# Kernel tuning notes

Measured on AMD Instinct MI355X. Metric: run time of the kernel, lower is better.

## Reference

```python
import jax, jax.numpy as jnp
import numpy as np

N_NODES = 50000
N_EDGES = 800000
D = 256
VOCAB = 50000
N_ETYPES = 3
N_STEPS = 5
N_GRAPHS = 64


def setup_inputs() -> dict:
    key = jax.random.key(0)
    ks = jax.random.split(key, 16)
    s = 1.0 / np.sqrt(D)
    return {
        "x": jax.random.randint(ks[0], (N_NODES,), 0, VOCAB),
        "src": jax.random.randint(ks[1], (N_EDGES,), 0, N_NODES),
        "dst": jax.random.randint(ks[2], (N_EDGES,), 0, N_NODES),
        "etypes": jax.random.randint(ks[3], (N_EDGES,), 0, N_ETYPES),
        "seg_ids": jnp.sort(jax.random.randint(ks[4], (N_NODES,), 0, N_GRAPHS)),
        "num_graphs": N_GRAPHS,
        "emb": jax.random.normal(ks[5], (VOCAB, D), jnp.float32),
        "W_msg": jax.random.normal(ks[6], (N_ETYPES, D, D), jnp.float32) * s,
        "b_msg": jax.random.normal(ks[7], (N_ETYPES, D), jnp.float32) * s,
        "w_ih": jax.random.normal(ks[8], (3 * D, D), jnp.float32) * s,
        "w_hh": jax.random.normal(ks[9], (3 * D, D), jnp.float32) * s,
        "b_ih": jax.random.normal(ks[10], (3 * D,), jnp.float32) * s,
        "b_hh": jax.random.normal(ks[11], (3 * D,), jnp.float32) * s,
        "gate_w": jax.random.normal(ks[12], (D, 1), jnp.float32) * s,
        "gate_b": jax.random.normal(ks[13], (1,), jnp.float32) * s,
    }


def _gru_cell(a, h, w_ih, w_hh, b_ih, b_hh):
    # a, h: [N, D]; gates: [N, 3D]
    gi = a @ w_ih.T + b_ih
    gh = h @ w_hh.T + b_hh
    i_r, i_z, i_n = jnp.split(gi, 3, axis=-1)
    h_r, h_z, h_n = jnp.split(gh, 3, axis=-1)
    r = jax.nn.sigmoid(i_r + h_r)
    z = jax.nn.sigmoid(i_z + h_z)
    n = jnp.tanh(i_n + r * h_n)
    return (1.0 - z) * n + z * h


def reference(x, src, dst, etypes, seg_ids, num_graphs, emb, W_msg, b_msg,
              w_ih, w_hh, b_ih, b_hh, gate_w, gate_b):
    # Embedding lookup (dropout is identity in eval mode)
    h = emb[x]  # [N, D]

    # GatedGraphConv: n_steps of per-etype linear message + scatter-add + GRU
    for _ in range(N_STEPS):
        # per-node transform under every etype's weight: [n_etypes, N, D]
        t = jnp.einsum("nd,edf->enf", h, W_msg)
        msg = t[etypes, src] + b_msg[etypes]        # [E, D]
        a = jax.ops.segment_sum(msg, dst, num_segments=N_NODES)  # [N, D]
        h = _gru_cell(a, h, w_ih, w_hh, b_ih, b_hh)

    # GlobalAttentionPooling: gate score + segment softmax + weighted sum
    gate = (h @ gate_w + gate_b)[:, 0]  # [N]
    gmax = jax.ops.segment_max(gate, seg_ids, num_segments=num_graphs)
    e = jnp.exp(gate - gmax[seg_ids])
    denom = jax.ops.segment_sum(e, seg_ids, num_segments=num_graphs)
    alpha = e / denom[seg_ids]  # [N]
    out = jax.ops.segment_sum(h * alpha[:, None], seg_ids, num_segments=num_graphs)
    return out  # [num_graphs, D]
```

## Files before the change

### kernel.cpp

```cpp
#include <hip/hip_runtime.h>
#include <hip/hip_bf16.h>
#include <stdint.h>

#define N_NODESC 50000
#define NPAD     50048
#define NPAD2    50176
#define N_EDGESC 800000
#define DIM      256
#define DIM3     768
#define NSTEPS   5
#define NGRAPH   64

typedef __attribute__((ext_vector_type(4))) float  f32x4;
typedef __attribute__((ext_vector_type(8))) short  short8;
typedef __attribute__((ext_vector_type(4))) unsigned short u16x4;
typedef __attribute__((ext_vector_type(4))) _Float16 f16x4;

__device__ float          g_hf[(size_t)NPAD * DIM];
__device__ unsigned short g_ah[(size_t)NPAD2 * 512];
__device__ unsigned short g_p [(size_t)NPAD2 * DIM3];
__device__ _Float16       g_gates[(size_t)NPAD2 * 1024];
__device__ unsigned short g_Wc[DIM * DIM3];
__device__ unsigned short g_WC2[1024 * 512];
__device__ float          g_biasC[1024];
__device__ int            g_cnt[NPAD2 * 4];
__device__ int            g_rowoff[N_NODESC + 1];
__device__ int            g_cur[N_NODESC];
__device__ unsigned       g_eidx[N_EDGESC];
__device__ int            g_bsum[256];
__device__ int            g_boff[256];
__device__ float          g_gate[N_NODESC];
__device__ int            g_soff[NGRAPH + 1];
__device__ float          g_gmax[NGRAPH];
__device__ float          g_gden[NGRAPH];

__device__ __forceinline__ float bf2f(unsigned short u) {
  unsigned x = ((unsigned)u) << 16;
  return __builtin_bit_cast(float, x);
}
__device__ __forceinline__ unsigned short f2bf(float f) {
  unsigned u = __builtin_bit_cast(unsigned, f);
  u += 0x7fffu + ((u >> 16) & 1u);
  return (unsigned short)(u >> 16);
}
__device__ __forceinline__ float sigm(float x) { return 1.0f / (1.0f + expf(-x)); }

__device__ __forceinline__ void async16(const void* g, void* l) {
  __builtin_amdgcn_global_load_lds(
      (const __attribute__((address_space(1))) unsigned int*)g,
      (__attribute__((address_space(3))) unsigned int*)l, 16, 0, 0);
}


__global__ void k_zero_cnt() {
  int i = blockIdx.x * 256 + threadIdx.x;
  g_cnt[i] = 0;
}

__global__ void k_prep_w(const float* __restrict__ Wmsg, const float* __restrict__ wih,
                         const float* __restrict__ whh, const float* __restrict__ bih,
                         const float* __restrict__ bhh) {
  int i = blockIdx.x * 256 + threadIdx.x;
  if (i < 196608) {
    int f = i / 768, j = i - f * 768;
    int e = j >> 8, d = j & 255;
    g_Wc[i] = f2bf(Wmsg[(e << 16) + (d << 8) + f]);
  } else if (i < 720896) {
    int t = i - 196608;
    int c = t >> 9, k = t & 511;
    float v;
    if (c < 512)       v = (k < 256) ? wih[c * 256 + k] : whh[c * 256 + (k - 256)];
    else if (c < 768)  v = (k < 256) ? wih[c * 256 + k] : 0.f;
    else               v = (k < 256) ? 0.f : whh[(c - 256) * 256 + (k - 256)];
    g_WC2[t] = f2bf(v);
  } else if (i < 721920) {
    int c = i - 720896;
    float v;
    if (c < 512)      v = bih[c] + bhh[c];
    else if (c < 768) v = bih[c];
    else              v = bhh[c - 256];
    g_biasC[c] = v;
  }
}

__global__ void k_embed(const int* __restrict__ x, const float* __restrict__ emb) {
  int i = blockIdx.x * 256 + threadIdx.x;
  int n = i >> 6, t = i & 63;
  if (n >= N_NODESC) return;
  float4 v = *(const float4*)(emb + (size_t)x[n] * DIM + t * 4);
  *(float4*)(g_hf + (size_t)n * DIM + t * 4) = v;
  u16x4 b = {f2bf(v.x), f2bf(v.y), f2bf(v.z), f2bf(v.w)};
  *(u16x4*)(g_ah + (size_t)n * 512 + 256 + t * 4) = b;
}

__global__ void k_count(const int* __restrict__ dst, const int* __restrict__ et) {
  int e = blockIdx.x * 256 + threadIdx.x;
  if (e >= N_EDGESC) return;
  atomicAdd(&g_cnt[dst[e] * 4 + et[e]], 1);
}

__global__ void k_scan1() {
  __shared__ int lds[256];
  int n = blockIdx.x * 256 + threadIdx.x;
  int deg = (n < N_NODESC) ? (g_cnt[n * 4] + g_cnt[n * 4 + 1] + g_cnt[n * 4 + 2]) : 0;
  lds[threadIdx.x] = deg;
  __syncthreads();
  for (int o = 128; o > 0; o >>= 1) {
    if (threadIdx.x < o) lds[threadIdx.x] += lds[threadIdx.x + o];
    __syncthreads();
  }
  if (threadIdx.x == 0) g_bsum[blockIdx.x] = lds[0];
}

__global__ void k_scan2() {
  __shared__ int lds[256];
  int t = threadIdx.x;
  int v = (t < 196) ? g_bsum[t] : 0;
  lds[t] = v;
  __syncthreads();
  for (int o = 1; o < 256; o <<= 1) {
    int u = (t >= o) ? lds[t - o] : 0;
    __syncthreads();
    lds[t] += u;
    __syncthreads();
  }
  if (t < 196) g_boff[t] = lds[t] - v;
}

__global__ void k_scan3() {
  __shared__ int lds[256];
  int n = blockIdx.x * 256 + threadIdx.x;
  int t = threadIdx.x;
  int deg = (n < N_NODESC) ? (g_cnt[n * 4] + g_cnt[n * 4 + 1] + g_cnt[n * 4 + 2]) : 0;
  lds[t] = deg;
  __syncthreads();
  for (int o = 1; o < 256; o <<= 1) {
    int u = (t >= o) ? lds[t - o] : 0;
    __syncthreads();
    lds[t] += u;
    __syncthreads();
  }
  if (n < N_NODESC) {
    int off = g_boff[blockIdx.x] + lds[t] - deg;
    g_rowoff[n] = off;
    g_cur[n] = off;
  }
  if (n == N_NODESC - 1) g_rowoff[N_NODESC] = g_boff[blockIdx.x] + lds[t];
}

__global__ void k_fill(const int* __restrict__ src, const int* __restrict__ dst,
                       const int* __restrict__ et) {
  int e = blockIdx.x * 256 + threadIdx.x;
  if (e >= N_EDGESC) return;
  int p = atomicAdd(&g_cur[dst[e]], 1);
  g_eidx[p] = (((unsigned)src[e]) << 2) | (unsigned)et[e];
}

__global__ void k_segoff(const int* __restrict__ seg) {
  int n = blockIdx.x * 256 + threadIdx.x;
  if (n >= N_NODESC) return;
  int g = seg[n];
  int gp = (n == 0) ? -1 : seg[n - 1];
  for (int t = gp + 1; t <= g; ++t) g_soff[t] = n;
  if (n == N_NODESC - 1)
    for (int t = g + 1; t <= NGRAPH; ++t) g_soff[t] = N_NODESC;
}


#define ACC_ET(hv, et)                                                        \
  {                                                                           \
    float x0 = bf2f(hv[0]), x1 = bf2f(hv[1]), x2 = bf2f(hv[2]), x3 = bf2f(hv[3]); \
    if (et == 0)      { a0[0] += x0; a0[1] += x1; a0[2] += x2; a0[3] += x3; } \
    else if (et == 1) { a1[0] += x0; a1[1] += x1; a1[2] += x2; a1[3] += x3; } \
    else              { a2[0] += x0; a2[1] += x1; a2[2] += x2; a2[3] += x3; } \
  }

__global__ __launch_bounds__(256) void k_agg() {
  int node = blockIdx.x * 4 + (threadIdx.x >> 6);
  int lane = threadIdx.x & 63;
  if (node >= N_NODESC) return;
  float a0[4] = {0.f, 0.f, 0.f, 0.f};
  float a1[4] = {0.f, 0.f, 0.f, 0.f};
  float a2[4] = {0.f, 0.f, 0.f, 0.f};
  int s = g_rowoff[node], e = g_rowoff[node + 1];
  int i = s;
  for (; i + 4 <= e; i += 4) {
    unsigned v0 = g_eidx[i], v1 = g_eidx[i + 1], v2 = g_eidx[i + 2], v3 = g_eidx[i + 3];
    u16x4 hv0 = *(const u16x4*)(g_ah + (size_t)(v0 >> 2) * 512 + 256 + lane * 4);
    u16x4 hv1 = *(const u16x4*)(g_ah + (size_t)(v1 >> 2) * 512 + 256 + lane * 4);
    u16x4 hv2 = *(const u16x4*)(g_ah + (size_t)(v2 >> 2) * 512 + 256 + lane * 4);
    u16x4 hv3 = *(const u16x4*)(g_ah + (size_t)(v3 >> 2) * 512 + 256 + lane * 4);
    int e0 = (int)(v0 & 3u), e1 = (int)(v1 & 3u), e2 = (int)(v2 & 3u), e3 = (int)(v3 & 3u);
    ACC_ET(hv0, e0);
    ACC_ET(hv1, e1);
    ACC_ET(hv2, e2);
    ACC_ET(hv3, e3);
  }
  for (; i < e; ++i) {
    unsigned v = g_eidx[i];
    u16x4 hv = *(const u16x4*)(g_ah + (size_t)(v >> 2) * 512 + 256 + lane * 4);
    int et = (int)(v & 3u);
    ACC_ET(hv, et);
  }
  size_t base = (size_t)node * DIM3 + lane * 4;
  u16x4 o0 = {f2bf(a0[0]), f2bf(a0[1]), f2bf(a0[2]), f2bf(a0[3])};
  u16x4 o1 = {f2bf(a1[0]), f2bf(a1[1]), f2bf(a1[2]), f2bf(a1[3])};
  u16x4 o2 = {f2bf(a2[0]), f2bf(a2[1]), f2bf(a2[2]), f2bf(a2[3])};
  *(u16x4*)(g_p + base)       = o0;
  *(u16x4*)(g_p + base + 256) = o1;
  *(u16x4*)(g_p + base + 512) = o2;
}

__global__ __launch_bounds__(256) void k_gemm0(const float* __restrict__ bmsg) {
  constexpr int K = DIM3;
  __shared__ unsigned short lA[128 * 64];
  __shared__ unsigned short lB[128 * 64];
  const int tx = threadIdx.x;
  const int lane = tx & 63;
  const int wave = tx >> 6;
  const int wr = wave >> 1, wc = wave & 1;
  const int bid = blockIdx.x + blockIdx.y * 2;
  const int xcd = bid & 7, ii = bid >> 3;
  const int tileM = (xcd * 49 + (ii >> 1)) * 128;
  const int tileN = (ii & 1) * 128;

  f32x4 acc[4][4];
#pragma unroll
  for (int m = 0; m < 4; ++m)
#pragma unroll
    for (int n = 0; n < 4; ++n) {
      acc[m][n][0] = 0.f; acc[m][n][1] = 0.f; acc[m][n][2] = 0.f; acc[m][n][3] = 0.f;
    }

  const int f = lane & 15, q = lane >> 4, xr = f & 7;

  int srow[4], scg[4];
#pragma unroll
  for (int i = 0; i < 4; ++i) {
    int byteo = i * 4096 + tx * 16;
    srow[i] = byteo >> 7;
    scg[i] = ((byteo >> 4) & 7) ^ (srow[i] & 7);
  }

  for (int k0 = 0; k0 < K; k0 += 64) {
#pragma unroll
    for (int i = 0; i < 4; ++i) {
      int byteo = i * 4096 + tx * 16;
      async16((const void*)(g_p + (size_t)(tileM + srow[i]) * K + k0 + scg[i] * 8),
              (void*)((char*)lA + byteo));
      async16((const void*)(g_Wc + (size_t)(tileN + srow[i]) * K + k0 + scg[i] * 8),
              (void*)((char*)lB + byteo));
    }
    __syncthreads();
#pragma unroll
    for (int kk = 0; kk < 2; ++kk) {
      short8 af[4], bfr[4];
#pragma unroll
      for (int m = 0; m < 4; ++m)
        af[m] = *(const short8*)((const char*)lA +
                 (wr * 64 + m * 16 + f) * 128 + (((kk * 4 + q) ^ xr) * 16));
#pragma unroll
      for (int n = 0; n < 4; ++n)
        bfr[n] = *(const short8*)((const char*)lB +
                 (wc * 64 + n * 16 + f) * 128 + (((kk * 4 + q) ^ xr) * 16));
#pragma unroll
      for (int m = 0; m < 4; ++m)
#pragma unroll
        for (int n = 0; n < 4; ++n)
          acc[m][n] = __builtin_amdgcn_mfma_f32_16x16x32_bf16(af[m], bfr[n], acc[m][n], 0, 0, 0);
    }
    __syncthreads();
  }

#pragma unroll
  for (int m = 0; m < 4; ++m) {
    int row0 = tileM + wr * 64 + m * 16 + q * 4;
#pragma unroll
    for (int n = 0; n < 4; ++n) {
      int col = tileN + wc * 64 + n * 16 + f;
      f32x4 v = acc[m][n];
#pragma unroll
      for (int r = 0; r < 4; ++r) {
        int row = row0 + r;
        const int* c = g_cnt + (size_t)row * 4;
        float val = v[r] + c[0] * bmsg[col] + c[1] * bmsg[256 + col] + c[2] * bmsg[512 + col];
        g_ah[(size_t)row * 512 + col] = f2bf(val);
      }
    }
  }
}

__global__ __launch_bounds__(256) void k_gemmC() {
  constexpr int K = 512;
  __shared__ unsigned short lA[128 * 64];
  __shared__ unsigned short lB[128 * 64];
  const int tx = threadIdx.x;
  const int lane = tx & 63;
  const int wave = tx >> 6;
  const int wr = wave >> 1, wc = wave & 1;
  const int bid = blockIdx.x + blockIdx.y * 8;
  const int xcd = bid & 7, ii = bid >> 3;
  const int tileM = (xcd * 49 + (ii >> 3)) * 128;
  const int tileN = (ii & 7) * 128;

  f32x4 acc[4][4];
#pragma unroll
  for (int m = 0; m < 4; ++m)
#pragma unroll
    for (int n = 0; n < 4; ++n) {
      acc[m][n][0] = 0.f; acc[m][n][1] = 0.f; acc[m][n][2] = 0.f; acc[m][n][3] = 0.f;
    }

  const int f = lane & 15, q = lane >> 4, xr = f & 7;

  int srow[4], scg[4];
#pragma unroll
  for (int i = 0; i < 4; ++i) {
    int byteo = i * 4096 + tx * 16;
    srow[i] = byteo >> 7;
    scg[i] = ((byteo >> 4) & 7) ^ (srow[i] & 7);
  }

  for (int k0 = 0; k0 < K; k0 += 64) {
#pragma unroll
    for (int i = 0; i < 4; ++i) {
      int byteo = i * 4096 + tx * 16;
      async16((const void*)(g_ah + (size_t)(tileM + srow[i]) * K + k0 + scg[i] * 8),
              (void*)((char*)lA + byteo));
      async16((const void*)(g_WC2 + (size_t)(tileN + srow[i]) * K + k0 + scg[i] * 8),
              (void*)((char*)lB + byteo));
    }
    __syncthreads();
#pragma unroll
    for (int kk = 0; kk < 2; ++kk) {
      short8 af[4], bfr[4];
#pragma unroll
      for (int m = 0; m < 4; ++m)
        af[m] = *(const short8*)((const char*)lA +
                 (wr * 64 + m * 16 + f) * 128 + (((kk * 4 + q) ^ xr) * 16));
#pragma unroll
      for (int n = 0; n < 4; ++n)
        bfr[n] = *(const short8*)((const char*)lB +
                 (wc * 64 + n * 16 + f) * 128 + (((kk * 4 + q) ^ xr) * 16));
#pragma unroll
      for (int m = 0; m < 4; ++m)
#pragma unroll
        for (int n = 0; n < 4; ++n)
          acc[m][n] = __builtin_amdgcn_mfma_f32_16x16x32_bf16(af[m], bfr[n], acc[m][n], 0, 0, 0);
    }
    __syncthreads();
  }

#pragma unroll
  for (int m = 0; m < 4; ++m) {
    int row0 = tileM + wr * 64 + m * 16 + q * 4;
#pragma unroll
    for (int n = 0; n < 4; ++n) {
      int col = tileN + wc * 64 + n * 16 + f;
      float bs = g_biasC[col];
#pragma unroll
      for (int r = 0; r < 4; ++r)
        g_gates[(size_t)(row0 + r) * 1024 + col] = (_Float16)(acc[m][n][r] + bs);
    }
  }
}

template <int LAST>
__global__ void k_gru(const float* __restrict__ gw, const float* __restrict__ gb) {
  int i = blockIdx.x * 256 + threadIdx.x;
  int n = i >> 6, t = (i & 63) * 4;
  if (n >= N_NODESC) return;
  size_t bg = (size_t)n * 1024 + t;
  size_t b1 = (size_t)n * DIM + t;
  f16x4 rz_r = *(const f16x4*)(g_gates + bg);
  f16x4 rz_z = *(const f16x4*)(g_gates + bg + 256);
  f16x4 in4  = *(const f16x4*)(g_gates + bg + 512);
  f16x4 hn4  = *(const f16x4*)(g_gates + bg + 768);
  float4 h = *(const float4*)(g_hf + b1);
  float4 o;
#pragma unroll
  for (int j = 0; j < 4; ++j) {
    float r = sigm((float)rz_r[j]);
    float z = sigm((float)rz_z[j]);
    float nn = tanhf((float)in4[j] + r * (float)hn4[j]);
    float hj = (j == 0) ? h.x : (j == 1) ? h.y : (j == 2) ? h.z : h.w;
    float oj = (1.f - z) * nn + z * hj;
    if (j == 0) o.x = oj; else if (j == 1) o.y = oj; else if (j == 2) o.z = oj; else o.w = oj;
  }
  *(float4*)(g_hf + b1) = o;
  u16x4 ob = {f2bf(o.x), f2bf(o.y), f2bf(o.z), f2bf(o.w)};
  *(u16x4*)(g_ah + (size_t)n * 512 + 256 + t) = ob;
  if (LAST) {
    float4 w = *(const float4*)(gw + t);
    float p = o.x * w.x + o.y * w.y + o.z * w.z + o.w * w.w;
    for (int off = 32; off > 0; off >>= 1) p += __shfl_xor(p, off);
    if ((threadIdx.x & 63) == 0) g_gate[n] = p + gb[0];
  }
}


__global__ void k_segred() {
  int g = blockIdx.x, t = threadIdx.x;
  __shared__ float red[256];
  int s = g_soff[g], e = g_soff[g + 1];
  float m = -3.4e38f;
  for (int n = s + t; n < e; n += 256) m = fmaxf(m, g_gate[n]);
  red[t] = m;
  __syncthreads();
  for (int o = 128; o > 0; o >>= 1) {
    if (t < o) red[t] = fmaxf(red[t], red[t + o]);
    __syncthreads();
  }
  m = red[0];
  __syncthreads();
  float sm = 0.f;
  for (int n = s + t; n < e; n += 256) sm += expf(g_gate[n] - m);
  red[t] = sm;
  __syncthreads();
  for (int o = 128; o > 0; o >>= 1) {
    if (t < o) red[t] += red[t + o];
    __syncthreads();
  }
  if (t == 0) {
    g_gmax[g] = m;
    g_gden[g] = (e > s && red[0] != 0.f) ? red[0] : 1.f;
  }
}

__global__ void k_zero_out(float* __restrict__ out) {
  out[blockIdx.x * 256 + threadIdx.x] = 0.f;
}

__global__ __launch_bounds__(256) void k_poolacc(const int* __restrict__ seg,
                                                 float* __restrict__ out) {
  __shared__ int   segL[128];
  __shared__ float alphaL[128];
  int base = blockIdx.x * 128;
  int t = threadIdx.x;
  if (t < 128) {
    int n = base + t;
    if (n < N_NODESC) {
      int g = seg[n];
      segL[t] = g;
      alphaL[t] = expf(g_gate[n] - g_gmax[g]) / g_gden[g];
    } else {
      segL[t] = -1;
    }
  }
  __syncthreads();
  float acc = 0.f;
  int gcur = segL[0];
  for (int j = 0; j < 128; ++j) {
    int gs = segL[j];
    if (gs < 0) break;
    if (gs != gcur) {
      atomicAdd(out + (size_t)gcur * DIM + t, acc);
      acc = 0.f;
      gcur = gs;
    }
    acc += alphaL[j] * g_hf[(size_t)(base + j) * DIM + t];
  }
  if (gcur >= 0) atomicAdd(out + (size_t)gcur * DIM + t, acc);
}


extern "C" void kernel_launch(void* const* d_in, const int* in_sizes, int n_in,
                              void* d_out, int out_size, void* d_ws, size_t ws_size,
                              hipStream_t stream) {
  const int* x = (const int*)d_in[0];
  const int* src = (const int*)d_in[1];
  const int* dst = (const int*)d_in[2];
  const int* ety = (const int*)d_in[3];
  const int* seg = (const int*)d_in[4];
  const float* emb = (const float*)d_in[6];
  const float* Wmsg = (const float*)d_in[7];
  const float* bmsg = (const float*)d_in[8];
  const float* wih = (const float*)d_in[9];
  const float* whh = (const float*)d_in[10];
  const float* bih = (const float*)d_in[11];
  const float* bhh = (const float*)d_in[12];
  const float* gw = (const float*)d_in[13];
  const float* gb = (const float*)d_in[14];
  float* out = (float*)d_out;

  k_zero_cnt<<<NPAD2 * 4 / 256, 256, 0, stream>>>();
  k_prep_w<<<2820, 256, 0, stream>>>(Wmsg, wih, whh, bih, bhh);
  k_embed<<<12500, 256, 0, stream>>>(x, emb);
  k_count<<<(N_EDGESC + 255) / 256, 256, 0, stream>>>(dst, ety);
  k_scan1<<<196, 256, 0, stream>>>();
  k_scan2<<<1, 256, 0, stream>>>();
  k_scan3<<<196, 256, 0, stream>>>();
  k_fill<<<(N_EDGESC + 255) / 256, 256, 0, stream>>>(src, dst, ety);
  k_segoff<<<196, 256, 0, stream>>>(seg);

  for (int s = 0; s < NSTEPS; ++s) {
    k_agg<<<12500, 256, 0, stream>>>();
    k_gemm0<<<dim3(2, 392), 256, 0, stream>>>(bmsg);
    k_gemmC<<<dim3(8, 392), 256, 0, stream>>>();
    if (s < NSTEPS - 1)
      k_gru<0><<<12500, 256, 0, stream>>>(nullptr, nullptr);
    else
      k_gru<1><<<12500, 256, 0, stream>>>(gw, gb);
  }

  k_segred<<<NGRAPH, 256, 0, stream>>>();
  k_zero_out<<<NGRAPH, 256, 0, stream>>>(out);
  k_poolacc<<<391, 256, 0, stream>>>(seg, out);
}
```

Before: 1.515 ms.

## Fuse GRU elementwise into gate GEMM epilogue with double-buffered hidden state

The weight matrix rows are reordered so that each 256-column N-tile holds the r, z, i_n and h_n gates for the same 64 hidden dimensions. The GRU nonlinearity and state update can then run directly in the GEMM epilogue, which removes the fp16 gates buffer write and read and the separate GRU kernel. The bf16 hidden copy is ping-ponged between two column slots so the next state can be written while other tiles still read the current one. The gate score dot product moves to a separate small kernel after the loop. The trade-offs are a larger per-block tile (2x16 accumulators, launch_bounds 256,1) with lower occupancy, and scattered fp32 h reads and writes in the epilogue.

```diff
diff --git a/kernel.cpp b/kernel.cpp
--- a/kernel.cpp
+++ b/kernel.cpp
@@ -14,15 +14,12 @@
 typedef __attribute__((ext_vector_type(4))) float  f32x4;
 typedef __attribute__((ext_vector_type(8))) short  short8;
 typedef __attribute__((ext_vector_type(4))) unsigned short u16x4;
-typedef __attribute__((ext_vector_type(4))) _Float16 f16x4;
-
-__device__ float          g_hf[(size_t)NPAD * DIM];
-__device__ unsigned short g_ah[(size_t)NPAD2 * 512];
+
+__device__ float          g_hf[(size_t)NPAD2 * DIM];
+__device__ unsigned short g_ah[(size_t)NPAD2 * 768];
 __device__ unsigned short g_p [(size_t)NPAD2 * DIM3];
-__device__ _Float16       g_gates[(size_t)NPAD2 * 1024];
 __device__ unsigned short g_Wc[DIM * DIM3];
-__device__ unsigned short g_WC2[1024 * 512];
-__device__ float          g_biasC[1024];
+__device__ unsigned short g_WC3[1024 * 512];
 __device__ int            g_cnt[NPAD2 * 4];
 __device__ int            g_rowoff[N_NODESC + 1];
 __device__ int            g_cur[N_NODESC];
@@ -58,8 +55,7 @@
 }
 
 __global__ void k_prep_w(const float* __restrict__ Wmsg, const float* __restrict__ wih,
-                         const float* __restrict__ whh, const float* __restrict__ bih,
-                         const float* __restrict__ bhh) {
+                         const float* __restrict__ whh) {
   int i = blockIdx.x * 256 + threadIdx.x;
   if (i < 196608) {
     int f = i / 768, j = i - f * 768;
@@ -67,19 +63,14 @@
     g_Wc[i] = f2bf(Wmsg[(e << 16) + (d << 8) + f]);
   } else if (i < 720896) {
     int t = i - 196608;
-    int c = t >> 9, k = t & 511;
+    int c3 = t >> 9, k = t & 511;
+    int g = c3 >> 8, rem = c3 & 255, p = rem >> 6, d = g * 64 + (rem & 63);
     float v;
-    if (c < 512)       v = (k < 256) ? wih[c * 256 + k] : whh[c * 256 + (k - 256)];
-    else if (c < 768)  v = (k < 256) ? wih[c * 256 + k] : 0.f;
-    else               v = (k < 256) ? 0.f : whh[(c - 256) * 256 + (k - 256)];
-    g_WC2[t] = f2bf(v);
-  } else if (i < 721920) {
-    int c = i - 720896;
-    float v;
-    if (c < 512)      v = bih[c] + bhh[c];
-    else if (c < 768) v = bih[c];
-    else              v = bhh[c - 256];
-    g_biasC[c] = v;
+    if (p == 0) { int rw = d;       v = (k < 256) ? wih[rw * 256 + k] : whh[rw * 256 + k - 256]; }
+    else if (p == 1) { int rw = 256 + d; v = (k < 256) ? wih[rw * 256 + k] : whh[rw * 256 + k - 256]; }
+    else if (p == 2) { int rw = 512 + d; v = (k < 256) ? wih[rw * 256 + k] : 0.f; }
+    else { int rw = 512 + d; v = (k < 256) ? 0.f : whh[rw * 256 + k - 256]; }
+    g_WC3[t] = f2bf(v);
   }
 }
 
@@ -90,7 +81,7 @@
   float4 v = *(const float4*)(emb + (size_t)x[n] * DIM + t * 4);
   *(float4*)(g_hf + (size_t)n * DIM + t * 4) = v;
   u16x4 b = {f2bf(v.x), f2bf(v.y), f2bf(v.z), f2bf(v.w)};
-  *(u16x4*)(g_ah + (size_t)n * 512 + 256 + t * 4) = b;
+  *(u16x4*)(g_ah + (size_t)n * 768 + 256 + t * 4) = b;
 }
 
 __global__ void k_count(const int* __restrict__ dst, const int* __restrict__ et) {
@@ -175,7 +166,7 @@
     else              { a2[0] += x0; a2[1] += x1; a2[2] += x2; a2[3] += x3; } \
   }
 
-__global__ __launch_bounds__(256) void k_agg() {
+__global__ __launch_bounds__(256) void k_agg(int hoff) {
   int node = blockIdx.x * 4 + (threadIdx.x >> 6);
   int lane = threadIdx.x & 63;
   if (node >= N_NODESC) return;
@@ -186,10 +177,10 @@
   int i = s;
   for (; i + 4 <= e; i += 4) {
     unsigned v0 = g_eidx[i], v1 = g_eidx[i + 1], v2 = g_eidx[i + 2], v3 = g_eidx[i + 3];
-    u16x4 hv0 = *(const u16x4*)(g_ah + (size_t)(v0 >> 2) * 512 + 256 + lane * 4);
-    u16x4 hv1 = *(const u16x4*)(g_ah + (size_t)(v1 >> 2) * 512 + 256 + lane * 4);
-    u16x4 hv2 = *(const u16x4*)(g_ah + (size_t)(v2 >> 2) * 512 + 256 + lane * 4);
-    u16x4 hv3 = *(const u16x4*)(g_ah + (size_t)(v3 >> 2) * 512 + 256 + lane * 4);
+    u16x4 hv0 = *(const u16x4*)(g_ah + (size_t)(v0 >> 2) * 768 + hoff + lane * 4);
+    u16x4 hv1 = *(const u16x4*)(g_ah + (size_t)(v1 >> 2) * 768 + hoff + lane * 4);
+    u16x4 hv2 = *(const u16x4*)(g_ah + (size_t)(v2 >> 2) * 768 + hoff + lane * 4);
+    u16x4 hv3 = *(const u16x4*)(g_ah + (size_t)(v3 >> 2) * 768 + hoff + lane * 4);
     int e0 = (int)(v0 & 3u), e1 = (int)(v1 & 3u), e2 = (int)(v2 & 3u), e3 = (int)(v3 & 3u);
     ACC_ET(hv0, e0);
     ACC_ET(hv1, e1);
@@ -198,7 +189,7 @@
   }
   for (; i < e; ++i) {
     unsigned v = g_eidx[i];
-    u16x4 hv = *(const u16x4*)(g_ah + (size_t)(v >> 2) * 512 + 256 + lane * 4);
+    u16x4 hv = *(const u16x4*)(g_ah + (size_t)(v >> 2) * 768 + hoff + lane * 4);
     int et = (int)(v & 3u);
     ACC_ET(hv, et);
   }
@@ -284,118 +275,101 @@
         int row = row0 + r;
         const int* c = g_cnt + (size_t)row * 4;
         float val = v[r] + c[0] * bmsg[col] + c[1] * bmsg[256 + col] + c[2] * bmsg[512 + col];
-        g_ah[(size_t)row * 512 + col] = f2bf(val);
+        g_ah[(size_t)row * 768 + col] = f2bf(val);
       }
     }
   }
 }
 
-__global__ __launch_bounds__(256) void k_gemmC() {
-  constexpr int K = 512;
+__global__ __launch_bounds__(256, 1) void k_gemmCG(const float* __restrict__ bih,
+                                                   const float* __restrict__ bhh,
+                                                   int hcur, int hnxt) {
   __shared__ unsigned short lA[128 * 64];
-  __shared__ unsigned short lB[128 * 64];
+  __shared__ unsigned short lB[256 * 64];
   const int tx = threadIdx.x;
   const int lane = tx & 63;
-  const int wave = tx >> 6;
-  const int wr = wave >> 1, wc = wave & 1;
-  const int bid = blockIdx.x + blockIdx.y * 8;
+  const int w = tx >> 6;
+  const int bid = blockIdx.x + blockIdx.y * 4;
   const int xcd = bid & 7, ii = bid >> 3;
-  const int tileM = (xcd * 49 + (ii >> 3)) * 128;
-  const int tileN = (ii & 7) * 128;
-
-  f32x4 acc[4][4];
-#pragma unroll
-  for (int m = 0; m < 4; ++m)
-#pragma unroll
-    for (int n = 0; n < 4; ++n) {
+  const int tileM = (xcd * 49 + (ii >> 2)) * 128;
+  const int g = ii & 3;
+  const int f = lane & 15, q = lane >> 4, xr = f & 7;
+
+  f32x4 acc[2][16];
+#pragma unroll
+  for (int m = 0; m < 2; ++m)
+#pragma unroll
+    for (int n = 0; n < 16; ++n) {
       acc[m][n][0] = 0.f; acc[m][n][1] = 0.f; acc[m][n][2] = 0.f; acc[m][n][3] = 0.f;
     }
 
-  const int f = lane & 15, q = lane >> 4, xr = f & 7;
-
-  int srow[4], scg[4];
-#pragma unroll
-  for (int i = 0; i < 4; ++i) {
-    int byteo = i * 4096 + tx * 16;
-    srow[i] = byteo >> 7;
-    scg[i] = ((byteo >> 4) & 7) ^ (srow[i] & 7);
-  }
-
-  for (int k0 = 0; k0 < K; k0 += 64) {
+  for (int k0 = 0; k0 < 512; k0 += 64) {
+    const int colbase = (k0 < 256) ? k0 : hcur + (k0 - 256);
 #pragma unroll
     for (int i = 0; i < 4; ++i) {
       int byteo = i * 4096 + tx * 16;
-      async16((const void*)(g_ah + (size_t)(tileM + srow[i]) * K + k0 + scg[i] * 8),
+      int row = byteo >> 7;
+      int cg = ((byteo >> 4) & 7) ^ (row & 7);
+      async16((const void*)(g_ah + (size_t)(tileM + row) * 768 + colbase + cg * 8),
               (void*)((char*)lA + byteo));
-      async16((const void*)(g_WC2 + (size_t)(tileN + srow[i]) * K + k0 + scg[i] * 8),
+    }
+#pragma unroll
+    for (int i = 0; i < 8; ++i) {
+      int byteo = i * 4096 + tx * 16;
+      int row = byteo >> 7;
+      int cg = ((byteo >> 4) & 7) ^ (row & 7);
+      async16((const void*)(g_WC3 + (size_t)(g * 256 + row) * 512 + k0 + cg * 8),
               (void*)((char*)lB + byteo));
     }
     __syncthreads();
 #pragma unroll
     for (int kk = 0; kk < 2; ++kk) {
-      short8 af[4], bfr[4];
-#pragma unroll
-      for (int m = 0; m < 4; ++m)
-        af[m] = *(const short8*)((const char*)lA +
-                 (wr * 64 + m * 16 + f) * 128 + (((kk * 4 + q) ^ xr) * 16));
-#pragma unroll
-      for (int n = 0; n < 4; ++n)
-        bfr[n] = *(const short8*)((const char*)lB +
-                 (wc * 64 + n * 16 + f) * 128 + (((kk * 4 + q) ^ xr) * 16));
-#pragma unroll
-      for (int m = 0; m < 4; ++m)
-#pragma unroll
-        for (int n = 0; n < 4; ++n)
-          acc[m][n] = __builtin_amdgcn_mfma_f32_16x16x32_bf16(af[m], bfr[n], acc[m][n], 0, 0, 0);
-    }
-    __syncthreads();
-  }
-
-#pragma unroll
-  for (int m = 0; m < 4; ++m) {
-    int row0 = tileM + wr * 64 + m * 16 + q * 4;
-#pragma unroll
-    for (int n = 0; n < 4; ++n) {
-      int col = tileN + wc * 64 + n * 16 + f;
-      float bs = g_biasC[col];
-#pragma unroll
-      for (int r = 0; r < 4; ++r)
-        g_gates[(size_t)(row0 + r) * 1024 + col] = (_Float16)(acc[m][n][r] + bs);
-    }
-  }
-}
-
-template <int LAST>
-__global__ void k_gru(const float* __restrict__ gw, const float* __restrict__ gb) {
-  int i = blockIdx.x * 256 + threadIdx.x;
-  int n = i >> 6, t = (i & 63) * 4;
-  if (n >= N_NODESC) return;
-  size_t bg = (size_t)n * 1024 + t;
-  size_t b1 = (size_t)n * DIM + t;
-  f16x4 rz_r = *(const f16x4*)(g_gates + bg);
-  f16x4 rz_z = *(const f16x4*)(g_gates + bg + 256);
-  f16x4 in4  = *(const f16x4*)(g_gates + bg + 512);
-  f16x4 hn4  = *(const f16x4*)(g_gates + bg + 768);
-  float4 h = *(const float4*)(g_hf + b1);
-  float4 o;
-#pragma unroll
-  for (int j = 0; j < 4; ++j) {
-    float r = sigm((float)rz_r[j]);
-    float z = sigm((float)rz_z[j]);
-    float nn = tanhf((float)in4[j] + r * (float)hn4[j]);
-    float hj = (j == 0) ? h.x : (j == 1) ? h.y : (j == 2) ? h.z : h.w;
-    float oj = (1.f - z) * nn + z * hj;
-    if (j == 0) o.x = oj; else if (j == 1) o.y = oj; else if (j == 2) o.z = oj; else o.w = oj;
-  }
-  *(float4*)(g_hf + b1) = o;
-  u16x4 ob = {f2bf(o.x), f2bf(o.y), f2bf(o.z), f2bf(o.w)};
-  *(u16x4*)(g_ah + (size_t)n * 512 + 256 + t) = ob;
-  if (LAST) {
-    float4 w = *(const float4*)(gw + t);
-    float p = o.x * w.x + o.y * w.y + o.z * w.z + o.w * w.w;
-    for (int off = 32; off > 0; off >>= 1) p += __shfl_xor(p, off);
-    if ((threadIdx.x & 63) == 0) g_gate[n] = p + gb[0];
-  }
+      int coff = ((kk * 4 + q) ^ xr) * 16;
+      short8 af0 = *(const short8*)((const char*)lA + (w * 32 + f) * 128 + coff);
+      short8 af1 = *(const short8*)((const char*)lA + (w * 32 + 16 + f) * 128 + coff);
+#pragma unroll
+      for (int n = 0; n < 16; ++n) {
+        short8 b = *(const short8*)((const char*)lB + (n * 16 + f) * 128 + coff);
+        acc[0][n] = __builtin_amdgcn_mfma_f32_16x16x32_bf16(af0, b, acc[0][n], 0, 0, 0);
+        acc[1][n] = __builtin_amdgcn_mfma_f32_16x16x32_bf16(af1, b, acc[1][n], 0, 0, 0);
+      }
+    }
+    __syncthreads();
+  }
+
+#pragma unroll
+  for (int m = 0; m < 2; ++m) {
+#pragma unroll
+    for (int j = 0; j < 4; ++j) {
+      int d = g * 64 + j * 16 + f;
+      float bR = bih[d] + bhh[d];
+      float bZ = bih[256 + d] + bhh[256 + d];
+      float bN = bih[512 + d];
+      float bH = bhh[512 + d];
+#pragma unroll
+      for (int r = 0; r < 4; ++r) {
+        int row = tileM + w * 32 + m * 16 + q * 4 + r;
+        float rr = sigm(acc[m][j][r] + bR);
+        float zz = sigm(acc[m][4 + j][r] + bZ);
+        float nn = tanhf(acc[m][8 + j][r] + bN + rr * (acc[m][12 + j][r] + bH));
+        float ho = g_hf[(size_t)row * DIM + d];
+        float o = (1.f - zz) * nn + zz * ho;
+        g_hf[(size_t)row * DIM + d] = o;
+        g_ah[(size_t)row * 768 + hnxt + d] = f2bf(o);
+      }
+    }
+  }
+}
+
+__global__ void k_gate(const float* __restrict__ gw, const float* __restrict__ gb) {
+  int node = blockIdx.x * 4 + (threadIdx.x >> 6);
+  int lane = threadIdx.x & 63;
+  if (node >= N_NODESC) return;
+  float4 h = *(const float4*)(g_hf + (size_t)node * DIM + lane * 4);
+  float4 w = *(const float4*)(gw + lane * 4);
+  float p = h.x * w.x + h.y * w.y + h.z * w.z + h.w * w.w;
+  for (int o = 32; o > 0; o >>= 1) p += __shfl_xor(p, o);
+  if (lane == 0) g_gate[node] = p + gb[0];
 }
 
 
@@ -484,7 +458,7 @@
   float* out = (float*)d_out;
 
   k_zero_cnt<<<NPAD2 * 4 / 256, 256, 0, stream>>>();
-  k_prep_w<<<2820, 256, 0, stream>>>(Wmsg, wih, whh, bih, bhh);
+  k_prep_w<<<2816, 256, 0, stream>>>(Wmsg, wih, whh);
   k_embed<<<12500, 256, 0, stream>>>(x, emb);
   k_count<<<(N_EDGESC + 255) / 256, 256, 0, stream>>>(dst, ety);
   k_scan1<<<196, 256, 0, stream>>>();
@@ -494,15 +468,14 @@
   k_segoff<<<196, 256, 0, stream>>>(seg);
 
   for (int s = 0; s < NSTEPS; ++s) {
-    k_agg<<<12500, 256, 0, stream>>>();
+    int hcur = 256 + (s & 1) * 256;
+    int hnxt = 256 + ((s + 1) & 1) * 256;
+    k_agg<<<12500, 256, 0, stream>>>(hcur);
     k_gemm0<<<dim3(2, 392), 256, 0, stream>>>(bmsg);
-    k_gemmC<<<dim3(8, 392), 256, 0, stream>>>();
-    if (s < NSTEPS - 1)
-      k_gru<0><<<12500, 256, 0, stream>>>(nullptr, nullptr);
-    else
-      k_gru<1><<<12500, 256, 0, stream>>>(gw, gb);
-  }
-
+    k_gemmCG<<<dim3(4, 392), 256, 0, stream>>>(bih, bhh, hcur, hnxt);
+  }
+
+  k_gate<<<12500, 256, 0, stream>>>(gw, gb);
   k_segred<<<NGRAPH, 256, 0, stream>>>();
   k_zero_out<<<NGRAPH, 256, 0, stream>>>(out);
   k_poolacc<<<391, 256, 0, stream>>>(seg, out);
```

Result: slower. 1.735 ms (+14.5%).
